# Kernel tuning notes

Hardware: AMD Instinct MI355X
Metric: run time of the kernel (lower is better)

## Reference

```python
import jax, jax.numpy as jnp
import numpy as np

C, NPC, DF, H, DO, EPC = 5, 400, 64, 256, 64, 12800  # categories, nodes/cat, feat, hidden, out, edges/cat
N = C * NPC


def _gcn(x, ei, ew, W, b):
    # GCNConv with edge weights + self loops (fill=1), symmetric normalization.
    n = x.shape[0]
    sl = jnp.arange(n)
    row = jnp.concatenate([ei[0], sl])
    col = jnp.concatenate([ei[1], sl])
    w = jnp.concatenate([ew, jnp.ones((n,), x.dtype)])
    deg = jax.ops.segment_sum(w, col, num_segments=n)
    dis = jnp.where(deg > 0, 1.0 / jnp.sqrt(deg), 0.0)
    norm = dis[row] * w * dis[col]                      # [e+n]
    h = x @ W                                           # [n, dout]
    out = jax.ops.segment_sum(h[row] * norm[:, None], col, num_segments=n)
    return out + b


def setup_inputs() -> dict:
    key = jax.random.key(0)
    ks = jax.random.split(key, 9)
    return {
        "x": jax.random.normal(ks[0], (C, NPC, DF), jnp.float32),
        "edge_weight": jax.random.uniform(ks[1], (C, EPC), jnp.float32),
        "W1": jax.random.normal(ks[2], (C, DF, H), jnp.float32) / np.sqrt(DF),
        "b1": jax.random.normal(ks[3], (C, H), jnp.float32) * 0.01,
        "W2": jax.random.normal(ks[4], (C, H, DO), jnp.float32) / np.sqrt(H),
        "b2": jax.random.normal(ks[5], (C, DO), jnp.float32) * 0.01,
        "W_att": jax.random.normal(ks[6], (2 * DO, 1), jnp.float32) / np.sqrt(2 * DO),
        "b_att": jax.random.normal(ks[7], (1,), jnp.float32) * 0.01,
        "edge_index": jax.random.randint(ks[8], (C, 2, EPC), 0, NPC, jnp.int64),
    }


def reference(x, edge_weight, W1, b1, W2, b2, W_att, b_att, edge_index):
    # ReconstructorHGNN: per-category GCN -> relu -> GCN (hetero edge types are intra-category only)
    h1 = jax.nn.relu(jax.vmap(_gcn)(x, edge_index, edge_weight, W1, b1))   # [C, NPC, H]
    h2 = jax.vmap(_gcn)(h1, edge_index, edge_weight, W2, b2)               # [C, NPC, DO]
    all_feat = h2.reshape(N, DO)                                           # cat over categories
    # Full-connect upper-triangular graph (u < v)
    iu, iv = jnp.triu_indices(N, k=1)                                      # E = N*(N-1)/2
    # LinearAttention: Linear(concat(x_u, x_v)) == x_u @ Wa + x_v @ Wb + b
    Wa, Wb = W_att[:DO], W_att[DO:]
    logits = all_feat[iu] @ Wa + all_feat[iv] @ Wb + b_att                 # [E, 1]
    m = jnp.mean(logits, axis=0)
    s = jnp.std(logits, axis=0, ddof=1)                                    # torch.std is unbiased
    return jax.nn.sigmoid((logits - m) / s)
```

## Files before the change

### kernel.cpp

```cpp
#include <hip/hip_runtime.h>
#include <math.h>

#define C    5
#define NPC  400
#define DF   64
#define HH   256
#define DOUT 64
#define EPC  12800
#define NN   (C*NPC)
#define NE   (C*EPC)

__global__ void deg_kernel(const float* __restrict__ ew, const int* __restrict__ ei,
                           float* __restrict__ deg) {
    int idx = blockIdx.x*256 + threadIdx.x;
    if (idx >= NE) return;
    int c = idx / EPC, e = idx % EPC;
    int col = ei[(size_t)c*2*EPC + EPC + e];
    atomicAdd(&deg[c*NPC + col], ew[(size_t)c*EPC + e]);
}

__global__ void adj_kernel(const float* __restrict__ ew, const int* __restrict__ ei,
                           const float* __restrict__ deg, float* __restrict__ Amat) {
    int idx = blockIdx.x*256 + threadIdx.x;
    if (idx < NE) {
        int c = idx / EPC, e = idx % EPC;
        const int* row = ei + (size_t)c*2*EPC;
        int r  = row[e];
        int cc = row[EPC + e];
        float w  = ew[(size_t)c*EPC + e];
        float dr = rsqrtf(deg[c*NPC + r]  + 1.0f);
        float dc = rsqrtf(deg[c*NPC + cc] + 1.0f);
        atomicAdd(&Amat[(size_t)c*NPC*NPC + (size_t)cc*NPC + r], dr*w*dc);
    }
    if (idx < NN) {
        int c = idx / NPC, n = idx % NPC;
        atomicAdd(&Amat[(size_t)c*NPC*NPC + (size_t)n*NPC + n], 1.0f/(deg[idx] + 1.0f));
    }
}

template<int M, int K, int N2, int BIAS, int RELU>
__global__ __launch_bounds__(256) void gemm_tiled(const float* __restrict__ A,
        const float* __restrict__ B, const float* __restrict__ bias,
        float* __restrict__ out) {
    __shared__ float As[16][68];
    __shared__ float Bs[16][68];
    const int c  = blockIdx.z;
    const int m0 = blockIdx.x << 6, n0 = blockIdx.y << 6;
    const float* Ab = A + (size_t)c*M*K;
    const float* Bb = B + (size_t)c*K*N2;
    const int tid = threadIdx.x;
    const int tx = tid & 15, ty = tid >> 4;
    const int lrow = tid >> 2, lk4 = (tid & 3) << 2;
    const int lkb = tid >> 4, lcol4 = (tid & 15) << 2;
    float acc[4][4] = {};
    for (int k0 = 0; k0 < K; k0 += 16) {
        float4 a4 = make_float4(0.f, 0.f, 0.f, 0.f);
        int gr = m0 + lrow;
        if (gr < M) a4 = *(const float4*)(Ab + (size_t)gr*K + k0 + lk4);
        As[lk4+0][lrow] = a4.x; As[lk4+1][lrow] = a4.y;
        As[lk4+2][lrow] = a4.z; As[lk4+3][lrow] = a4.w;
        *(float4*)&Bs[lkb][lcol4] = *(const float4*)(Bb + (size_t)(k0+lkb)*N2 + n0 + lcol4);
        __syncthreads();
        #pragma unroll
        for (int kk = 0; kk < 16; ++kk) {
            float4 av = *(float4*)&As[kk][ty << 2];
            float4 bv = *(float4*)&Bs[kk][tx << 2];
            acc[0][0] += av.x*bv.x; acc[0][1] += av.x*bv.y; acc[0][2] += av.x*bv.z; acc[0][3] += av.x*bv.w;
            acc[1][0] += av.y*bv.x; acc[1][1] += av.y*bv.y; acc[1][2] += av.y*bv.z; acc[1][3] += av.y*bv.w;
            acc[2][0] += av.z*bv.x; acc[2][1] += av.z*bv.y; acc[2][2] += av.z*bv.z; acc[2][3] += av.z*bv.w;
            acc[3][0] += av.w*bv.x; acc[3][1] += av.w*bv.y; acc[3][2] += av.w*bv.z; acc[3][3] += av.w*bv.w;
        }
        __syncthreads();
    }
    #pragma unroll
    for (int i = 0; i < 4; ++i) {
        int gr = m0 + (ty << 2) + i;
        if (gr >= M) break;
        float4 o = make_float4(acc[i][0], acc[i][1], acc[i][2], acc[i][3]);
        if (BIAS) {
            const float* bb = bias + c*N2 + n0 + (tx << 2);
            o.x += bb[0]; o.y += bb[1]; o.z += bb[2]; o.w += bb[3];
        }
        if (RELU) {
            o.x = fmaxf(o.x, 0.f); o.y = fmaxf(o.y, 0.f);
            o.z = fmaxf(o.z, 0.f); o.w = fmaxf(o.w, 0.f);
        }
        *(float4*)(out + (size_t)c*M*N2 + (size_t)gr*N2 + n0 + (tx << 2)) = o;
    }
}

__global__ void wprep(const float* __restrict__ W2, const float* __restrict__ Watt,
                      const float* __restrict__ b2, float* __restrict__ wa2,
                      float* __restrict__ wb2, float* __restrict__ cab) {
    int c = blockIdx.x, k = threadIdx.x;
    const float* w2 = W2 + ((size_t)c*HH + k)*DOUT;
    float sa = 0.f, sb = 0.f;
    for (int d = 0; d < DOUT; ++d) { sa += w2[d]*Watt[d]; sb += w2[d]*Watt[DOUT+d]; }
    wa2[c*HH + k] = sa; wb2[c*HH + k] = sb;
    if (k < 2) {
        const float* bb = b2 + c*DOUT;
        const float* wv = Watt + k*DOUT;
        float s = 0.f;
        for (int d = 0; d < DOUT; ++d) s += bb[d]*wv[d];
        cab[k*C + c] = s;
    }
}

__global__ void tvec(const float* __restrict__ h1, const float* __restrict__ wa2,
                     const float* __restrict__ wb2, float* __restrict__ ta,
                     float* __restrict__ tb) {
    int w = blockIdx.x*4 + (threadIdx.x >> 6);
    int lane = threadIdx.x & 63;
    if (w >= NN) return;
    int c = w / NPC;
    const float* hr = h1 + (size_t)w*HH;
    const float* wa = wa2 + c*HH;
    const float* wb = wb2 + c*HH;
    float sa = 0.f, sb = 0.f;
    for (int d = lane; d < HH; d += 64) { float h = hr[d]; sa += h*wa[d]; sb += h*wb[d]; }
    for (int off = 32; off; off >>= 1) { sa += __shfl_down(sa, off); sb += __shfl_down(sb, off); }
    if (!lane) { ta[w] = sa; tb[w] = sb; }
}

__global__ void avbv(const float* __restrict__ Amat, const float* __restrict__ ta,
                     const float* __restrict__ tb, const float* __restrict__ cab,
                     float* __restrict__ av, float* __restrict__ bv) {
    int w = blockIdx.x*4 + (threadIdx.x >> 6);
    int lane = threadIdx.x & 63;
    if (w >= NN) return;
    int c = w / NPC, n = w % NPC;
    const float* Ar = Amat + (size_t)c*NPC*NPC + (size_t)n*NPC;
    const float* tac = ta + c*NPC;
    const float* tbc = tb + c*NPC;
    float sa = 0.f, sb = 0.f;
    for (int m = lane; m < NPC; m += 64) { float a = Ar[m]; sa += a*tac[m]; sb += a*tbc[m]; }
    for (int off = 32; off; off >>= 1) { sa += __shfl_down(sa, off); sb += __shfl_down(sb, off); }
    if (!lane) { av[w] = sa + cab[c]; bv[w] = sb + cab[C + c]; }
}

__global__ void stats_kernel(const float* __restrict__ av, const float* __restrict__ bv,
                             const float* __restrict__ b_att, float* __restrict__ stats) {
    __shared__ double wred[5][4];
    __shared__ double wsum[4];
    int t = threadIdx.x;
    int lane = t & 63, wid = t >> 6;
    const int CH = 8;
    int lo = t*CH, hi = lo + CH; if (hi > NN) hi = NN; if (lo > NN) lo = NN;

    double sa1=0, sb1=0, sa2=0, sb2=0, csum=0;
    for (int i = lo; i < hi; ++i) {
        double a = av[i], b = bv[i];
        double wa = (double)(NN-1-i), wb = (double)i;
        sa1 += a*wa; sb1 += b*wb;
        sa2 += a*a*wa; sb2 += b*b*wb;
        csum += a;
    }
    double v0=sa1, v1=sb1, v2=sa2, v3=sb2;
    for (int off = 32; off; off >>= 1) {
        v0 += __shfl_down(v0, off); v1 += __shfl_down(v1, off);
        v2 += __shfl_down(v2, off); v3 += __shfl_down(v3, off);
    }
    if (!lane) { wred[0][wid]=v0; wred[1][wid]=v1; wred[2][wid]=v2; wred[3][wid]=v3; }
    double x = csum;
    for (int off = 1; off < 64; off <<= 1) {
        double y = __shfl_up(x, off);
        if (lane >= off) x += y;
    }
    if (lane == 63) wsum[wid] = x;
    __syncthreads();
    double woff = 0;
    for (int wI = 0; wI < wid; ++wI) woff += wsum[wI];
    double run = woff + x - csum;
    double ct = 0;
    for (int i = lo; i < hi; ++i) { ct += (double)bv[i]*run; run += (double)av[i]; }
    for (int off = 32; off; off >>= 1) ct += __shfl_down(ct, off);
    if (!lane) wred[4][wid] = ct;
    __syncthreads();
    if (t == 0) {
        double T0=0, T1=0, T2=0, T3=0, CT=0;
        for (int wI = 0; wI < 4; ++wI) {
            T0 += wred[0][wI]; T1 += wred[1][wI]; T2 += wred[2][wI];
            T3 += wred[3][wI]; CT += wred[4][wI];
        }
        double cc = (double)b_att[0];
        double P  = (double)NN*(double)(NN-1)/2.0;
        double S1 = T0 + T1 + cc*P;
        double S2 = T2 + T3 + 2.0*CT + 2.0*cc*S1 - cc*cc*P;
        double m  = S1/P;
        double var = (S2 - S1*S1/P)/(P - 1.0);
        stats[0] = (float)m;
        stats[1] = (float)sqrt(var);
    }
}

__global__ void pair_kernel(const float* __restrict__ av, const float* __restrict__ bv,
                            const float* __restrict__ b_att, const float* __restrict__ stats,
                            float* __restrict__ out) {
    int i = blockIdx.x;
    long off = (long)i*(NN-1) - ((long)i*(i-1))/2;
    float m = stats[0], s = stats[1];
    float inv = 1.0f/s;
    float ai = av[i] + b_att[0] - m;
    for (int j = i + 1 + threadIdx.x; j < NN; j += blockDim.x) {
        float z = (ai + bv[j]) * inv;
        out[off + (j - i - 1)] = 1.0f/(1.0f + __expf(-z));
    }
}

extern "C" void kernel_launch(void* const* d_in, const int* in_sizes, int n_in,
                              void* d_out, int out_size, void* d_ws, size_t ws_size,
                              hipStream_t stream) {
    const float* x    = (const float*)d_in[0];
    const float* ew   = (const float*)d_in[1];
    const float* W1   = (const float*)d_in[2];
    const float* b1   = (const float*)d_in[3];
    const float* W2   = (const float*)d_in[4];
    const float* b2   = (const float*)d_in[5];
    const float* Watt = (const float*)d_in[6];
    const float* batt = (const float*)d_in[7];
    const int*   ei   = (const int*)d_in[8];
    float* out = (float*)d_out;
    float* ws  = (float*)d_ws;

    float* Amat  = ws;
    float* deg   = Amat + 800000;
    float* xW    = deg  + 2000;
    float* h1    = xW   + 512000;
    float* wa2   = h1   + 512000;
    float* wb2   = wa2  + 1280;
    float* cab   = wb2  + 1280;
    float* ta    = cab  + 12;
    float* tb    = ta   + 2000;
    float* av    = tb   + 2000;
    float* bv    = av   + 2000;
    float* stats = bv   + 2000;

    hipMemsetAsync(Amat, 0, (size_t)(800000 + 2000)*sizeof(float), stream);

    deg_kernel<<<(NE + 255)/256, 256, 0, stream>>>(ew, ei, deg);
    adj_kernel<<<(NE + 255)/256, 256, 0, stream>>>(ew, ei, deg, Amat);

    gemm_tiled<NPC, DF,  HH, 0, 0><<<dim3(7, 4, C), 256, 0, stream>>>(x,    W1, nullptr, xW);
    gemm_tiled<NPC, NPC, HH, 1, 1><<<dim3(7, 4, C), 256, 0, stream>>>(Amat, xW, b1,      h1);

    wprep<<<C, 256, 0, stream>>>(W2, Watt, b2, wa2, wb2, cab);
    tvec<<<(NN + 3)/4, 256, 0, stream>>>(h1, wa2, wb2, ta, tb);
    avbv<<<(NN + 3)/4, 256, 0, stream>>>(Amat, ta, tb, cab, av, bv);

    stats_kernel<<<1, 256, 0, stream>>>(av, bv, batt, stats);
    pair_kernel<<<NN, 256, 0, stream>>>(av, bv, batt, stats, out);
}
```

Baseline: 141.0 us.

## Fuse wprep into adjacency kernel and fold tvec projection into second GEMM epilogue

Merges the W2·Watt precompute into the adjacency-build kernel, using one wavefront per row. The second GEMM no longer writes h1. Its epilogue applies bias and ReLU, projects onto wa2/wb2, and atomically accumulates into ta/tb. GEMM tiles shrink from 64 to 32 rows, giving more blocks for this small problem. The changes remove two launches and the h1 round trip, in exchange for atomics, a larger memset, and less reuse per tile.

```diff
diff --git a/kernel.cpp b/kernel.cpp
--- a/kernel.cpp
+++ b/kernel.cpp
@@ -19,8 +19,11 @@
     atomicAdd(&deg[c*NPC + col], ew[(size_t)c*EPC + e]);
 }
 
-__global__ void adj_kernel(const float* __restrict__ ew, const int* __restrict__ ei,
-                           const float* __restrict__ deg, float* __restrict__ Amat) {
+__global__ void adj_wprep_kernel(const float* __restrict__ ew, const int* __restrict__ ei,
+                                 const float* __restrict__ deg, const float* __restrict__ W2,
+                                 const float* __restrict__ Watt, const float* __restrict__ b2,
+                                 float* __restrict__ Amat, float* __restrict__ wa2,
+                                 float* __restrict__ wb2, float* __restrict__ cab) {
     int idx = blockIdx.x*256 + threadIdx.x;
     if (idx < NE) {
         int c = idx / EPC, e = idx % EPC;
@@ -36,90 +39,96 @@
         int c = idx / NPC, n = idx % NPC;
         atomicAdd(&Amat[(size_t)c*NPC*NPC + (size_t)n*NPC + n], 1.0f/(deg[idx] + 1.0f));
     }
-}
-
-template<int M, int K, int N2, int BIAS, int RELU>
-__global__ __launch_bounds__(256) void gemm_tiled(const float* __restrict__ A,
+    int W = blockIdx.x*4 + (threadIdx.x >> 6);
+    int lane = threadIdx.x & 63;
+    if (W < C*HH) {
+        int c = W / HH, k = W % HH;
+        float v  = W2[((size_t)c*HH + k)*DOUT + lane];
+        float sa = v*Watt[lane];
+        float sb = v*Watt[DOUT + lane];
+        for (int off = 32; off; off >>= 1) { sa += __shfl_down(sa, off); sb += __shfl_down(sb, off); }
+        if (!lane) { wa2[W] = sa; wb2[W] = sb; }
+    } else if (W < C*HH + 2*C) {
+        int j = W - C*HH;
+        int which = j / C, c = j % C;
+        float s = b2[c*DOUT + lane]*Watt[which*DOUT + lane];
+        for (int off = 32; off; off >>= 1) s += __shfl_down(s, off);
+        if (!lane) cab[which*C + c] = s;
+    }
+}
+
+template<int M, int K, int N2, int BIAS, int RELU, int FUSETAB>
+__global__ __launch_bounds__(256) void gemm32(const float* __restrict__ A,
         const float* __restrict__ B, const float* __restrict__ bias,
-        float* __restrict__ out) {
-    __shared__ float As[16][68];
+        float* __restrict__ out, const float* __restrict__ wa2,
+        const float* __restrict__ wb2, float* __restrict__ ta, float* __restrict__ tb) {
+    __shared__ float As[16][34];
     __shared__ float Bs[16][68];
     const int c  = blockIdx.z;
-    const int m0 = blockIdx.x << 6, n0 = blockIdx.y << 6;
+    const int m0 = blockIdx.x << 5, n0 = blockIdx.y << 6;
     const float* Ab = A + (size_t)c*M*K;
     const float* Bb = B + (size_t)c*K*N2;
     const int tid = threadIdx.x;
     const int tx = tid & 15, ty = tid >> 4;
-    const int lrow = tid >> 2, lk4 = (tid & 3) << 2;
+    const int lrowA = tid >> 3, lk2 = (tid & 7) << 1;
     const int lkb = tid >> 4, lcol4 = (tid & 15) << 2;
-    float acc[4][4] = {};
+    float acc[2][4] = {};
     for (int k0 = 0; k0 < K; k0 += 16) {
-        float4 a4 = make_float4(0.f, 0.f, 0.f, 0.f);
-        int gr = m0 + lrow;
-        if (gr < M) a4 = *(const float4*)(Ab + (size_t)gr*K + k0 + lk4);
-        As[lk4+0][lrow] = a4.x; As[lk4+1][lrow] = a4.y;
-        As[lk4+2][lrow] = a4.z; As[lk4+3][lrow] = a4.w;
+        float2 a2 = make_float2(0.f, 0.f);
+        int gr = m0 + lrowA;
+        if (gr < M) a2 = *(const float2*)(Ab + (size_t)gr*K + k0 + lk2);
+        As[lk2][lrowA] = a2.x; As[lk2+1][lrowA] = a2.y;
         *(float4*)&Bs[lkb][lcol4] = *(const float4*)(Bb + (size_t)(k0+lkb)*N2 + n0 + lcol4);
         __syncthreads();
         #pragma unroll
         for (int kk = 0; kk < 16; ++kk) {
-            float4 av = *(float4*)&As[kk][ty << 2];
+            float2 av = *(float2*)&As[kk][ty << 1];
             float4 bv = *(float4*)&Bs[kk][tx << 2];
             acc[0][0] += av.x*bv.x; acc[0][1] += av.x*bv.y; acc[0][2] += av.x*bv.z; acc[0][3] += av.x*bv.w;
             acc[1][0] += av.y*bv.x; acc[1][1] += av.y*bv.y; acc[1][2] += av.y*bv.z; acc[1][3] += av.y*bv.w;
-            acc[2][0] += av.z*bv.x; acc[2][1] += av.z*bv.y; acc[2][2] += av.z*bv.z; acc[2][3] += av.z*bv.w;
-            acc[3][0] += av.w*bv.x; acc[3][1] += av.w*bv.y; acc[3][2] += av.w*bv.z; acc[3][3] += av.w*bv.w;
         }
         __syncthreads();
     }
-    #pragma unroll
-    for (int i = 0; i < 4; ++i) {
-        int gr = m0 + (ty << 2) + i;
-        if (gr >= M) break;
-        float4 o = make_float4(acc[i][0], acc[i][1], acc[i][2], acc[i][3]);
-        if (BIAS) {
-            const float* bb = bias + c*N2 + n0 + (tx << 2);
-            o.x += bb[0]; o.y += bb[1]; o.z += bb[2]; o.w += bb[3];
-        }
-        if (RELU) {
-            o.x = fmaxf(o.x, 0.f); o.y = fmaxf(o.y, 0.f);
-            o.z = fmaxf(o.z, 0.f); o.w = fmaxf(o.w, 0.f);
-        }
-        *(float4*)(out + (size_t)c*M*N2 + (size_t)gr*N2 + n0 + (tx << 2)) = o;
-    }
-}
-
-__global__ void wprep(const float* __restrict__ W2, const float* __restrict__ Watt,
-                      const float* __restrict__ b2, float* __restrict__ wa2,
-                      float* __restrict__ wb2, float* __restrict__ cab) {
-    int c = blockIdx.x, k = threadIdx.x;
-    const float* w2 = W2 + ((size_t)c*HH + k)*DOUT;
-    float sa = 0.f, sb = 0.f;
-    for (int d = 0; d < DOUT; ++d) { sa += w2[d]*Watt[d]; sb += w2[d]*Watt[DOUT+d]; }
-    wa2[c*HH + k] = sa; wb2[c*HH + k] = sb;
-    if (k < 2) {
-        const float* bb = b2 + c*DOUT;
-        const float* wv = Watt + k*DOUT;
-        float s = 0.f;
-        for (int d = 0; d < DOUT; ++d) s += bb[d]*wv[d];
-        cab[k*C + c] = s;
-    }
-}
-
-__global__ void tvec(const float* __restrict__ h1, const float* __restrict__ wa2,
-                     const float* __restrict__ wb2, float* __restrict__ ta,
-                     float* __restrict__ tb) {
-    int w = blockIdx.x*4 + (threadIdx.x >> 6);
-    int lane = threadIdx.x & 63;
-    if (w >= NN) return;
-    int c = w / NPC;
-    const float* hr = h1 + (size_t)w*HH;
-    const float* wa = wa2 + c*HH;
-    const float* wb = wb2 + c*HH;
-    float sa = 0.f, sb = 0.f;
-    for (int d = lane; d < HH; d += 64) { float h = hr[d]; sa += h*wa[d]; sb += h*wb[d]; }
-    for (int off = 32; off; off >>= 1) { sa += __shfl_down(sa, off); sb += __shfl_down(sb, off); }
-    if (!lane) { ta[w] = sa; tb[w] = sb; }
+    if (FUSETAB) {
+        float pa0 = 0.f, pa1 = 0.f, pb0 = 0.f, pb1 = 0.f;
+        #pragma unroll
+        for (int j = 0; j < 4; ++j) {
+            int col = n0 + (tx << 2) + j;
+            float bj  = bias[c*N2 + col];
+            float waj = wa2[c*N2 + col];
+            float wbj = wb2[c*N2 + col];
+            float o0 = fmaxf(acc[0][j] + bj, 0.f);
+            float o1 = fmaxf(acc[1][j] + bj, 0.f);
+            pa0 += o0*waj; pa1 += o1*waj;
+            pb0 += o0*wbj; pb1 += o1*wbj;
+        }
+        #pragma unroll
+        for (int off = 1; off < 16; off <<= 1) {
+            pa0 += __shfl_xor(pa0, off); pa1 += __shfl_xor(pa1, off);
+            pb0 += __shfl_xor(pb0, off); pb1 += __shfl_xor(pb1, off);
+        }
+        if (tx == 0) {
+            int gr0 = m0 + (ty << 1);
+            if (gr0 < M)     { atomicAdd(&ta[c*M + gr0],     pa0); atomicAdd(&tb[c*M + gr0],     pb0); }
+            if (gr0 + 1 < M) { atomicAdd(&ta[c*M + gr0 + 1], pa1); atomicAdd(&tb[c*M + gr0 + 1], pb1); }
+        }
+    } else {
+        #pragma unroll
+        for (int i = 0; i < 2; ++i) {
+            int gr = m0 + (ty << 1) + i;
+            if (gr >= M) break;
+            float4 o = make_float4(acc[i][0], acc[i][1], acc[i][2], acc[i][3]);
+            if (BIAS) {
+                const float* bb = bias + c*N2 + n0 + (tx << 2);
+                o.x += bb[0]; o.y += bb[1]; o.z += bb[2]; o.w += bb[3];
+            }
+            if (RELU) {
+                o.x = fmaxf(o.x, 0.f); o.y = fmaxf(o.y, 0.f);
+                o.z = fmaxf(o.z, 0.f); o.w = fmaxf(o.w, 0.f);
+            }
+            *(float4*)(out + (size_t)c*M*N2 + (size_t)gr*N2 + n0 + (tx << 2)) = o;
+        }
+    }
 }
 
 __global__ void avbv(const float* __restrict__ Amat, const float* __restrict__ ta,
@@ -224,29 +233,27 @@
 
     float* Amat  = ws;
     float* deg   = Amat + 800000;
-    float* xW    = deg  + 2000;
-    float* h1    = xW   + 512000;
-    float* wa2   = h1   + 512000;
+    float* ta    = deg  + 2000;
+    float* tb    = ta   + 2000;
+    float* xW    = tb   + 2000;
+    float* wa2   = xW   + 512000;
     float* wb2   = wa2  + 1280;
     float* cab   = wb2  + 1280;
-    float* ta    = cab  + 12;
-    float* tb    = ta   + 2000;
-    float* av    = tb   + 2000;
+    float* av    = cab  + 12;
     float* bv    = av   + 2000;
     float* stats = bv   + 2000;
 
-    hipMemsetAsync(Amat, 0, (size_t)(800000 + 2000)*sizeof(float), stream);
+    hipMemsetAsync(ws, 0, (size_t)806000*sizeof(float), stream);
 
     deg_kernel<<<(NE + 255)/256, 256, 0, stream>>>(ew, ei, deg);
-    adj_kernel<<<(NE + 255)/256, 256, 0, stream>>>(ew, ei, deg, Amat);
-
-    gemm_tiled<NPC, DF,  HH, 0, 0><<<dim3(7, 4, C), 256, 0, stream>>>(x,    W1, nullptr, xW);
-    gemm_tiled<NPC, NPC, HH, 1, 1><<<dim3(7, 4, C), 256, 0, stream>>>(Amat, xW, b1,      h1);
-
-    wprep<<<C, 256, 0, stream>>>(W2, Watt, b2, wa2, wb2, cab);
-    tvec<<<(NN + 3)/4, 256, 0, stream>>>(h1, wa2, wb2, ta, tb);
+    adj_wprep_kernel<<<323, 256, 0, stream>>>(ew, ei, deg, W2, Watt, b2, Amat, wa2, wb2, cab);
+
+    gemm32<NPC, DF,  HH, 0, 0, 0><<<dim3(13, 4, C), 256, 0, stream>>>(x,    W1, nullptr, xW,
+                                                                      nullptr, nullptr, nullptr, nullptr);
+    gemm32<NPC, NPC, HH, 1, 1, 1><<<dim3(13, 4, C), 256, 0, stream>>>(Amat, xW, b1, nullptr,
+                                                                      wa2, wb2, ta, tb);
+
     avbv<<<(NN + 3)/4, 256, 0, stream>>>(Amat, ta, tb, cab, av, bv);
-
     stats_kernel<<<1, 256, 0, stream>>>(av, bv, batt, stats);
     pair_kernel<<<NN, 256, 0, stream>>>(av, bv, batt, stats, out);
 }
```

Result: faster. 128.8 us (-8.7%).
